# Kernel tuning notes

Hardware: AMD Instinct MI355X
Metric: run time of the kernel (lower is better)

Reference implementation:

```python
import jax, jax.numpy as jnp
import numpy as np


def _bce_logits(x, z):
    # numerically stable binary_cross_entropy_with_logits (elementwise)
    return jnp.maximum(x, 0.0) - x * z + jnp.log1p(jnp.exp(-jnp.abs(x)))


def _giou(b1, b2):
    # boxes in (cx, cy, w, h) format, mirrors bbox_iou(..., mode='giou')
    eps = 1e-9
    b1x1 = b1[..., 0] - b1[..., 2] / 2; b1y1 = b1[..., 1] - b1[..., 3] / 2
    b1x2 = b1[..., 0] + b1[..., 2] / 2; b1y2 = b1[..., 1] + b1[..., 3] / 2
    b2x1 = b2[..., 0] - b2[..., 2] / 2; b2y1 = b2[..., 1] - b2[..., 3] / 2
    b2x2 = b2[..., 0] + b2[..., 2] / 2; b2y2 = b2[..., 1] + b2[..., 3] / 2
    a1 = jnp.clip(b1x2 - b1x1, 0.0) * jnp.clip(b1y2 - b1y1, 0.0) + eps
    a2 = jnp.clip(b2x2 - b2x1, 0.0) * jnp.clip(b2y2 - b2y1, 0.0) + eps
    iw = jnp.clip(jnp.minimum(b1x2, b2x2) - jnp.maximum(b1x1, b2x1), 0.0)
    ih = jnp.clip(jnp.minimum(b1y2, b2y2) - jnp.maximum(b1y1, b2y1), 0.0)
    inter = iw * ih + eps
    union = a1 + a2 - inter + eps
    iou = inter / union
    cw = jnp.maximum(b1x2, b2x2) - jnp.minimum(b1x1, b2x1)
    ch = jnp.maximum(b1y2, b2y2) - jnp.minimum(b1y1, b2y1)
    carea = cw * ch + eps
    return iou - (carea - union) / carea


def setup_inputs() -> dict:
    key = jax.random.key(0)
    ks = jax.random.split(key, 8)
    N, A, S, nC, nM, G, H, W = 4, 3, 13, 80, 32, 16, 104, 104
    preds = jax.random.normal(ks[0], (N, A, S, S, 5 + nC + nM), jnp.float32) * 0.5
    prototypes = jax.random.normal(ks[1], (N, nM, H, W), jnp.float32)
    masks = (jax.random.uniform(ks[2], (N, G, H, W)) < 0.3).astype(jnp.float32)
    ii = jnp.arange(S)
    interior = (ii >= 2) & (ii <= 10)
    int2d = interior[:, None] & interior[None, :]
    obj = (jax.random.uniform(ks[3], (N, A, S, S)) < 0.06) & int2d
    obj = obj.at[:, 0, 6, 6].set(True)  # guarantee >= 1 object per image
    xy = jax.random.uniform(ks[4], (N, A, S, S, 2), minval=0.2, maxval=0.8)
    wh = jax.random.uniform(ks[5], (N, A, S, S, 2), minval=0.5, maxval=2.5)
    cls = jax.random.randint(ks[6], (N, A, S, S, 1), 0, nC).astype(jnp.float32)
    mid = jax.random.randint(ks[7], (N, A, S, S, 1), 0, G).astype(jnp.float32)
    target = jnp.concatenate([xy, wh, obj[..., None].astype(jnp.float32), cls, mid], axis=-1)
    anchors = jnp.array([[1.0, 1.5], [2.0, 2.5], [3.5, 3.0]], jnp.float32)
    return {"preds": preds, "target": target, "anchors": anchors,
            "prototypes": prototypes, "masks": masks,
            "num_classes": 80, "num_masks": 32}


def reference(preds, target, anchors, prototypes, masks, num_classes, num_masks):
    eps = 1e-9
    N, A, S = preds.shape[0], preds.shape[1], preds.shape[2]
    H, W = prototypes.shape[2], prototypes.shape[3]
    nC, nM = num_classes, num_masks
    dt = preds.dtype
    conf_t = target[..., 4]
    obj = conf_t == 1.0
    noobj = conf_t == 0.0
    objf = obj.astype(dt)
    noobjf = noobj.astype(dt)
    n_obj = objf.sum()
    n_noobj = noobjf.sum()
    conf_logit = preds[..., 4]
    noobj_loss = (_bce_logits(conf_logit, conf_t) * noobjf).sum() / n_noobj
    # ---- segmentation loss (dense masked equivalent of ragged per-instance crops) ----
    coeffs = jnp.tanh(preds[..., 5 + nC:5 + nC + nM])            # [N,A,S,S,M]
    inst = jnp.einsum('naijm,nmhw->naijhw', coeffs, prototypes)   # instance logits
    cols = jnp.arange(S, dtype=dt)
    # cells_to_boxes: normalized image coords, then scaled to prototype pixels
    bx = (target[..., 0] + cols[None, None, None, :]) / S * W
    by = (target[..., 1] + cols[None, None, :, None]) / S * H
    bw = target[..., 2] / S * W
    bh = target[..., 3] / S * H
    x1 = jnp.floor(bx - bw / 2).astype(jnp.int32)
    x2 = jnp.floor(bx + bw / 2).astype(jnp.int32)
    y1 = jnp.floor(by - bh / 2).astype(jnp.int32)
    y2 = jnp.floor(by + bh / 2).astype(jnp.int32)
    ids = jnp.clip(target[..., 6].astype(jnp.int32), 0, masks.shape[1] - 1)
    tm = masks[jnp.arange(N)[:, None, None, None], ids]           # [N,A,S,S,H,W]
    hh = jnp.arange(H)
    ww = jnp.arange(W)
    rm = ((hh >= y1[..., None]) & (hh < y2[..., None])).astype(dt)  # [N,A,S,S,H]
    cm = ((ww >= x1[..., None]) & (ww < x2[..., None])).astype(dt)  # [N,A,S,S,W]
    bce_el = _bce_logits(inst, tm)
    region_sum = jnp.einsum('naijhw,naijh,naijw->naij', bce_el, rm, cm)
    area = rm.sum(-1) * cm.sum(-1)
    valid = (area > 0) & obj
    seg_mean = jnp.where(valid, region_sum / jnp.maximum(area, 1.0), 0.0)
    segment_loss = seg_mean.sum() / (valid.astype(dt).sum() + eps)
    # ---- box / obj / class losses ----
    anch = anchors.reshape(1, A, 1, 1, 2)
    pred_box = jnp.concatenate([jax.nn.sigmoid(preds[..., 0:2]),
                                jnp.exp(preds[..., 2:4]) * anch], axis=-1)
    giou = _giou(pred_box, target[..., 0:4])                      # [N,A,S,S]
    obj_tgt = conf_t * jnp.clip(jax.lax.stop_gradient(giou), 0.0)
    obj_loss = (_bce_logits(conf_logit, obj_tgt) * objf).sum() / n_obj
    # note: original applies BCEWithLogits to sigmoid(xy) (double squash) - faithful
    xy_bce = (_bce_logits(jax.nn.sigmoid(preds[..., 0:2]), target[..., 0:2])
              * objf[..., None]).sum() / (n_obj * 2)
    twh = jnp.log(1e-16 + target[..., 2:4] / anch)
    wh_mse = (((preds[..., 2:4] - twh) ** 2) * objf[..., None]).sum() / (n_obj * 2)
    box_loss = xy_bce + wh_mse + ((1.0 - giou) * objf).sum() / n_obj
    logp = jax.nn.log_softmax(preds[..., 5:5 + nC], axis=-1)
    labels = target[..., 5].astype(jnp.int32)
    nll = -jnp.take_along_axis(logp, labels[..., None], axis=-1)[..., 0]
    class_loss = (nll * objf).sum() / n_obj
    box_l = 8.0 * box_loss
    obj_l = 2.0 * obj_loss
    noobj_l = 4.0 * noobj_loss
    cls_l = 1.0 * class_loss
    seg_l = 10.0 * segment_loss
    total = box_l + obj_l + noobj_l + cls_l + seg_l
    return jnp.stack([box_l, obj_l, noobj_l, cls_l, seg_l, total])
```

## Files before the change

kernel.cpp:

```cpp
#include <hip/hip_runtime.h>
#include <math.h>

#define N_  4
#define A_  3
#define S_  13
#define NC_ 80
#define NM_ 32
#define G_  16
#define H_  104
#define W_  104
#define CH_ (5 + NC_ + NM_)
#define HW_ (H_ * W_)
#define NCELL (N_ * A_ * S_ * S_)

#define MAIN_BLOCKS 64
#define PROW 16
#define P2_WAVES ((MAIN_BLOCKS - 8) * 4)
#define P2_K 10


__device__ __forceinline__ float bce_logits(float x, float z) {
    return fmaxf(x, 0.0f) - x * z + log1pf(expf(-fabsf(x)));
}

__device__ __forceinline__ float sigmoidf(float x) {
    return 1.0f / (1.0f + expf(-x));
}

__device__ __forceinline__ float readlane_f(float v, int l) {
    return __int_as_float(__builtin_amdgcn_readlane(__float_as_int(v), l));
}

__device__ __forceinline__ float giou_fn(float cx1, float cy1, float w1, float h1,
                                         float cx2, float cy2, float w2, float h2) {
    const float eps = 1e-9f;
    float b1x1 = cx1 - w1 * 0.5f, b1y1 = cy1 - h1 * 0.5f;
    float b1x2 = cx1 + w1 * 0.5f, b1y2 = cy1 + h1 * 0.5f;
    float b2x1 = cx2 - w2 * 0.5f, b2y1 = cy2 - h2 * 0.5f;
    float b2x2 = cx2 + w2 * 0.5f, b2y2 = cy2 + h2 * 0.5f;
    float a1 = fmaxf(b1x2 - b1x1, 0.0f) * fmaxf(b1y2 - b1y1, 0.0f) + eps;
    float a2 = fmaxf(b2x2 - b2x1, 0.0f) * fmaxf(b2y2 - b2y1, 0.0f) + eps;
    float iw = fmaxf(fminf(b1x2, b2x2) - fmaxf(b1x1, b2x1), 0.0f);
    float ih = fmaxf(fminf(b1y2, b2y2) - fmaxf(b1y1, b2y1), 0.0f);
    float inter = iw * ih + eps;
    float uni   = a1 + a2 - inter + eps;
    float iou   = inter / uni;
    float cw = fmaxf(b1x2, b2x2) - fminf(b1x1, b2x1);
    float ch = fmaxf(b1y2, b2y2) - fminf(b1y1, b2y1);
    float carea = cw * ch + eps;
    return iou - (carea - uni) / carea;
}

__device__ __forceinline__ void region_bounds_v(float t0, float t1, float t2, float t3,
                                                int i, int j,
                                                int& lox, int& loy, int& ncols, int& nrows) {
    float bx = (t0 + (float)j) * ((float)W_ / (float)S_);
    float by = (t1 + (float)i) * ((float)H_ / (float)S_);
    float bw = t2 * ((float)W_ / (float)S_);
    float bh = t3 * ((float)H_ / (float)S_);
    int x1 = (int)floorf(bx - bw * 0.5f);
    int x2 = (int)floorf(bx + bw * 0.5f);
    int y1 = (int)floorf(by - bh * 0.5f);
    int y2 = (int)floorf(by + bh * 0.5f);
    lox = max(x1, 0); loy = max(y1, 0);
    ncols = max(min(x2, W_) - lox, 0);
    nrows = max(min(y2, H_) - loy, 0);
}

__global__ __launch_bounds__(256) void yolo_fused_kernel(
    const float* __restrict__ preds,
    const float* __restrict__ target,
    const float* __restrict__ anchors,
    const float* __restrict__ protos,
    const float* __restrict__ masks,
    float* __restrict__ partials,
    unsigned int* __restrict__ ticket,
    float* __restrict__ out)
{
    const int b    = blockIdx.x;
    const int tid  = threadIdx.x;
    const int wav  = tid >> 6;
    const int lane = tid & 63;

    __shared__ float s_w[4][8];
    __shared__ float s_seg[4];
    __shared__ int   s_nv[4];
    __shared__ int   s_last;

    if (b < 8) {
        const int cell = b * 256 + tid;
        float v0 = 0.f, v1 = 0.f, v2 = 0.f, v3 = 0.f,
              v4 = 0.f, v5 = 0.f, v6 = 0.f, v7 = 0.f;

        if (cell < NCELL) {
            const int a = (cell / (S_ * S_)) % A_;
            const float* t = target + (size_t)cell * 7;
            const float* p = preds  + (size_t)cell * CH_;
            const float conf_t = t[4];
            const float x = p[4];

            if (conf_t == 0.0f) {
                v1 = 1.0f;
                v2 = bce_logits(x, 0.0f);
            } else if (conf_t == 1.0f) {
                v0 = 1.0f;
                float tx = t[0], ty = t[1], tw = t[2], th = t[3];
                float aw = anchors[a * 2 + 0], ah = anchors[a * 2 + 1];
                float sx = sigmoidf(p[0]);
                float sy = sigmoidf(p[1]);
                float pw = expf(p[2]) * aw;
                float ph = expf(p[3]) * ah;
                float giou = giou_fn(sx, sy, pw, ph, tx, ty, tw, th);
                v3 = bce_logits(x, fmaxf(giou, 0.0f));
                v4 = bce_logits(sx, tx) + bce_logits(sy, ty);
                float twl = logf(1e-16f + tw / aw);
                float thl = logf(1e-16f + th / ah);
                float dw = p[2] - twl, dh = p[3] - thl;
                v5 = dw * dw + dh * dh;
                v6 = 1.0f - giou;

                float mx = -1e30f;
                #pragma unroll 8
                for (int c = 0; c < NC_; ++c) mx = fmaxf(mx, p[5 + c]);
                float se = 0.0f;
                #pragma unroll 8
                for (int c = 0; c < NC_; ++c) se += expf(p[5 + c] - mx);
                int label = (int)t[5];
                v7 = (mx + logf(se)) - p[5 + label];
            }
        }

        #pragma unroll
        for (int o = 32; o > 0; o >>= 1) {
            v0 += __shfl_xor(v0, o, 64);  v1 += __shfl_xor(v1, o, 64);
            v2 += __shfl_xor(v2, o, 64);  v3 += __shfl_xor(v3, o, 64);
            v4 += __shfl_xor(v4, o, 64);  v5 += __shfl_xor(v5, o, 64);
            v6 += __shfl_xor(v6, o, 64);  v7 += __shfl_xor(v7, o, 64);
        }
        if ((tid & 63) == 0) {
            int w = tid >> 6;
            s_w[w][0] = v0; s_w[w][1] = v1; s_w[w][2] = v2; s_w[w][3] = v3;
            s_w[w][4] = v4; s_w[w][5] = v5; s_w[w][6] = v6; s_w[w][7] = v7;
        }
        __syncthreads();
        if (tid < 8) {
            partials[b * PROW + tid] =
                s_w[0][tid] + s_w[1][tid] + s_w[2][tid] + s_w[3][tid];
        }
        if (tid == 0) {
            partials[b * PROW + 8] = 0.0f;
            partials[b * PROW + 9] = 0.0f;
        }
    } else {
        const int gw = (b - 8) * 4 + wav;

        int   pc   = gw + lane * P2_WAVES;
        bool  in   = (lane < P2_K) && (pc < NCELL);
        float conf = 0.0f;
        int   lox = 0, loy = 0, ncols = 0, nrows = 0, idc = 0, parea = 0;
        if (in) {
            const float* t = target + (size_t)pc * 7;
            float t0 = t[0], t1 = t[1], t2 = t[2], t3 = t[3];
            conf = t[4];
            float t6 = t[6];
            region_bounds_v(t0, t1, t2, t3, (pc / S_) % S_, pc % S_,
                            lox, loy, ncols, nrows);
            parea = nrows * ncols;
            idc   = min(max((int)t6, 0), G_ - 1);
        }
        unsigned long long vmask = __ballot(in && conf == 1.0f && parea > 0);
        const int wave_nv = (int)__popcll(vmask);

        float wave_seg = 0.0f;
        while (vmask) {
            const int l = __ffsll(vmask) - 1;
            vmask &= vmask - 1;
            const int cell = gw + l * P2_WAVES;

            const int rlox = __builtin_amdgcn_readlane(lox,   l);
            const int rloy = __builtin_amdgcn_readlane(loy,   l);
            const int rnc  = __builtin_amdgcn_readlane(ncols, l);
            const int rnr  = __builtin_amdgcn_readlane(nrows, l);
            const int rid  = __builtin_amdgcn_readlane(idc,   l);
            const int rn   = cell / (A_ * S_ * S_);
            const int area = rnr * rnc;

            const float* p  = preds  + (size_t)cell * CH_;
            const float* tm = masks  + ((size_t)(rn * G_ + rid)) * HW_;
            const float* pr = protos + (size_t)rn * NM_ * HW_;

            float cv = 0.0f;
            if (lane < NM_) cv = tanhf(p[5 + NC_ + lane]);
            float cm[NM_];
            #pragma unroll
            for (int m = 0; m < NM_; ++m) cm[m] = readlane_f(cv, m);

            float lsum = 0.0f;
            for (int px = lane; px < area; px += 64) {
                int h = rloy + px / rnc;
                int w = rlox + px % rnc;
                int off = h * W_ + w;
                float inst = 0.0f;
                #pragma unroll
                for (int m = 0; m < NM_; ++m)
                    inst += cm[m] * pr[m * HW_ + off];
                lsum += bce_logits(inst, tm[off]);
            }

            #pragma unroll
            for (int o = 32; o > 0; o >>= 1) lsum += __shfl_xor(lsum, o, 64);
            if (lane == 0) wave_seg += lsum / (float)area;
        }

        if (lane == 0) { s_seg[wav] = wave_seg; s_nv[wav] = wave_nv; }
        __syncthreads();
        if (tid == 0) {
            partials[b * PROW + 8] = s_seg[0] + s_seg[1] + s_seg[2] + s_seg[3];
            partials[b * PROW + 9] =
                (float)(s_nv[0] + s_nv[1] + s_nv[2] + s_nv[3]);
        }
    }

    __syncthreads();
    if (tid == 0) {
        __threadfence();
        unsigned int old = atomicInc(ticket, MAIN_BLOCKS - 1u);
        s_last = (old == MAIN_BLOCKS - 2u) ? 1 : 0;
    }
    __syncthreads();
    if (!s_last) return;

    if (tid < 64) {
        __threadfence();
        const int t = tid;
        float s0 = 0.f, s1 = 0.f, s2 = 0.f, s3 = 0.f,
              s4 = 0.f, s5 = 0.f, s6 = 0.f, s7 = 0.f, s8 = 0.f, s9 = 0.f;
        if (t < 8) {
            s0 = partials[t * PROW + 0]; s1 = partials[t * PROW + 1];
            s2 = partials[t * PROW + 2]; s3 = partials[t * PROW + 3];
            s4 = partials[t * PROW + 4]; s5 = partials[t * PROW + 5];
            s6 = partials[t * PROW + 6]; s7 = partials[t * PROW + 7];
        }
        s8 = partials[t * PROW + 8];
        s9 = partials[t * PROW + 9];

        #pragma unroll
        for (int o = 32; o > 0; o >>= 1) {
            s0 += __shfl_xor(s0, o, 64);  s1 += __shfl_xor(s1, o, 64);
            s2 += __shfl_xor(s2, o, 64);  s3 += __shfl_xor(s3, o, 64);
            s4 += __shfl_xor(s4, o, 64);  s5 += __shfl_xor(s5, o, 64);
            s6 += __shfl_xor(s6, o, 64);  s7 += __shfl_xor(s7, o, 64);
            s8 += __shfl_xor(s8, o, 64);  s9 += __shfl_xor(s9, o, 64);
        }

        if (t == 0) {
            float n_obj   = s0;
            float n_noobj = s1;
            float noobj_loss = s2 / n_noobj;
            float obj_loss   = s3 / n_obj;
            float xy_bce     = s4 / (n_obj * 2.0f);
            float wh_mse     = s5 / (n_obj * 2.0f);
            float box_loss   = xy_bce + wh_mse + s6 / n_obj;
            float class_loss = s7 / n_obj;
            float seg_loss   = s8 / (s9 + 1e-9f);
            float box_l   = 8.0f * box_loss;
            float obj_l   = 2.0f * obj_loss;
            float noobj_l = 4.0f * noobj_loss;
            float cls_l   = 1.0f * class_loss;
            float seg_l   = 10.0f * seg_loss;
            out[0] = box_l;
            out[1] = obj_l;
            out[2] = noobj_l;
            out[3] = cls_l;
            out[4] = seg_l;
            out[5] = box_l + obj_l + noobj_l + cls_l + seg_l;
        }
    }
}

extern "C" void kernel_launch(void* const* d_in, const int* in_sizes, int n_in,
                              void* d_out, int out_size, void* d_ws, size_t ws_size,
                              hipStream_t stream) {
    const float* preds   = (const float*)d_in[0];
    const float* target  = (const float*)d_in[1];
    const float* anchors = (const float*)d_in[2];
    const float* protos  = (const float*)d_in[3];
    const float* masks   = (const float*)d_in[4];

    float* partials      = (float*)d_ws;
    unsigned int* ticket = (unsigned int*)(partials + MAIN_BLOCKS * PROW);
    float* out           = (float*)d_out;

    yolo_fused_kernel<<<MAIN_BLOCKS, 256, 0, stream>>>(preds, target, anchors,
                                                       protos, masks, partials,
                                                       ticket, out);
}
```

Baseline: 93.08 us.

## Spread segment-mask work over more blocks and prefetch mask coefficients before the loop

Raises the grid from 64 to 256 blocks, so each phase-2 wave handles at most 3 cells instead of 10, which spreads the per-object prototype GEMV work across more CUs. Mask coefficients (tanh of preds) for all candidate cells are loaded speculatively before the per-object loop, taking the dependent global load and tanh off the serial critical path. The final reducer now loops over 256 partial rows. The cost is more blocks that find no object and finish idle, some wasted speculative loads, and a longer final reduction.

```diff
diff --git a/kernel.cpp b/kernel.cpp
--- a/kernel.cpp
+++ b/kernel.cpp
@@ -13,10 +13,12 @@
 #define HW_ (H_ * W_)
 #define NCELL (N_ * A_ * S_ * S_)
 
-#define MAIN_BLOCKS 64
+#define MAIN_BLOCKS 256
+#define P1_BLOCKS 8
+#define P2_BLOCKS (MAIN_BLOCKS - P1_BLOCKS)
+#define P2_WAVES  (P2_BLOCKS * 4)
+#define P2_K 3
 #define PROW 16
-#define P2_WAVES ((MAIN_BLOCKS - 8) * 4)
-#define P2_K 10
 
 
 __device__ __forceinline__ float bce_logits(float x, float z) {
@@ -87,7 +89,7 @@
     __shared__ int   s_nv[4];
     __shared__ int   s_last;
 
-    if (b < 8) {
+    if (b < P1_BLOCKS) {
         const int cell = b * 256 + tid;
         float v0 = 0.f, v1 = 0.f, v2 = 0.f, v3 = 0.f,
               v4 = 0.f, v5 = 0.f, v6 = 0.f, v7 = 0.f;
@@ -96,26 +98,28 @@
             const int a = (cell / (S_ * S_)) % A_;
             const float* t = target + (size_t)cell * 7;
             const float* p = preds  + (size_t)cell * CH_;
-            const float conf_t = t[4];
-            const float x = p[4];
+            float tx = t[0], ty = t[1], tw = t[2], th = t[3];
+            float conf_t = t[4];
+            float t5 = t[5];
+            float p0 = p[0], p1 = p[1], p2 = p[2], p3 = p[3];
+            float x  = p[4];
 
             if (conf_t == 0.0f) {
                 v1 = 1.0f;
                 v2 = bce_logits(x, 0.0f);
             } else if (conf_t == 1.0f) {
                 v0 = 1.0f;
-                float tx = t[0], ty = t[1], tw = t[2], th = t[3];
                 float aw = anchors[a * 2 + 0], ah = anchors[a * 2 + 1];
-                float sx = sigmoidf(p[0]);
-                float sy = sigmoidf(p[1]);
-                float pw = expf(p[2]) * aw;
-                float ph = expf(p[3]) * ah;
+                float sx = sigmoidf(p0);
+                float sy = sigmoidf(p1);
+                float pw = expf(p2) * aw;
+                float ph = expf(p3) * ah;
                 float giou = giou_fn(sx, sy, pw, ph, tx, ty, tw, th);
                 v3 = bce_logits(x, fmaxf(giou, 0.0f));
                 v4 = bce_logits(sx, tx) + bce_logits(sy, ty);
                 float twl = logf(1e-16f + tw / aw);
                 float thl = logf(1e-16f + th / ah);
-                float dw = p[2] - twl, dh = p[3] - thl;
+                float dw = p2 - twl, dh = p3 - thl;
                 v5 = dw * dw + dh * dh;
                 v6 = 1.0f - giou;
 
@@ -125,7 +129,7 @@
                 float se = 0.0f;
                 #pragma unroll 8
                 for (int c = 0; c < NC_; ++c) se += expf(p[5 + c] - mx);
-                int label = (int)t[5];
+                int label = (int)t5;
                 v7 = (mx + logf(se)) - p[5 + label];
             }
         }
@@ -152,7 +156,7 @@
             partials[b * PROW + 9] = 0.0f;
         }
     } else {
-        const int gw = (b - 8) * 4 + wav;
+        const int gw = (b - P1_BLOCKS) * 4 + wav;
 
         int   pc   = gw + lane * P2_WAVES;
         bool  in   = (lane < P2_K) && (pc < NCELL);
@@ -168,6 +172,14 @@
             parea = nrows * ncols;
             idc   = min(max((int)t6, 0), G_ - 1);
         }
+        const int m    = lane & 31;
+        const int cA   = gw + (lane >> 5) * P2_WAVES;
+        float cf01 = tanhf(preds[(size_t)cA * CH_ + 5 + NC_ + m]);
+        const int c2   = gw + 2 * P2_WAVES;
+        float cf2  = 0.0f;
+        if (c2 < NCELL && lane < 32)
+            cf2 = tanhf(preds[(size_t)c2 * CH_ + 5 + NC_ + m]);
+
         unsigned long long vmask = __ballot(in && conf == 1.0f && parea > 0);
         const int wave_nv = (int)__popcll(vmask);
 
@@ -185,15 +197,15 @@
             const int rn   = cell / (A_ * S_ * S_);
             const int area = rnr * rnc;
 
-            const float* p  = preds  + (size_t)cell * CH_;
+            const float src  = (l == 2) ? cf2 : cf01;
+            const int   base = (l == 1) ? 32 : 0;
+            float cm[NM_];
+            #pragma unroll
+            for (int mm = 0; mm < NM_; ++mm)
+                cm[mm] = readlane_f(src, base + mm);
+
             const float* tm = masks  + ((size_t)(rn * G_ + rid)) * HW_;
             const float* pr = protos + (size_t)rn * NM_ * HW_;
-
-            float cv = 0.0f;
-            if (lane < NM_) cv = tanhf(p[5 + NC_ + lane]);
-            float cm[NM_];
-            #pragma unroll
-            for (int m = 0; m < NM_; ++m) cm[m] = readlane_f(cv, m);
 
             float lsum = 0.0f;
             for (int px = lane; px < area; px += 64) {
@@ -202,8 +214,8 @@
                 int off = h * W_ + w;
                 float inst = 0.0f;
                 #pragma unroll
-                for (int m = 0; m < NM_; ++m)
-                    inst += cm[m] * pr[m * HW_ + off];
+                for (int mm = 0; mm < NM_; ++mm)
+                    inst += cm[mm] * pr[mm * HW_ + off];
                 lsum += bce_logits(inst, tm[off]);
             }
 
@@ -241,8 +253,11 @@
             s4 = partials[t * PROW + 4]; s5 = partials[t * PROW + 5];
             s6 = partials[t * PROW + 6]; s7 = partials[t * PROW + 7];
         }
-        s8 = partials[t * PROW + 8];
-        s9 = partials[t * PROW + 9];
+        #pragma unroll
+        for (int r = t; r < MAIN_BLOCKS; r += 64) {
+            s8 += partials[r * PROW + 8];
+            s9 += partials[r * PROW + 9];
+        }
 
         #pragma unroll
         for (int o = 32; o > 0; o >>= 1) {
```

Result: slower. 95.38 us (+2.5%).
